# Optimization experiments

Hardware: AMD Instinct MI355X
Metric: run time of the kernel (lower is better)

## Reference

```python
import jax, jax.numpy as jnp
import numpy as np
from jax import lax

KH = KW = 3
STRIDE = 1
PAD = 1
B_COEF = 1.0
IN_CH = 64
OUT_CH = 64
C_LEN = 8
MLP_HIDDEN = 16


def setup_inputs() -> dict:
    key = jax.random.key(0)
    ks = jax.random.split(key, 8)
    IKK = IN_CH * KH * KW
    x = jax.random.normal(ks[0], (2, IN_CH, 32, 32), dtype=jnp.float32)
    c = jax.random.normal(ks[1], (2, C_LEN), dtype=jnp.float32)
    # static kernel [O, I*k*k] (xavier-uniform-ish)
    lim_k = float(np.sqrt(6.0 / (OUT_CH + IKK)))
    kernel = jax.random.uniform(ks[2], (OUT_CH, IKK), minval=-lim_k, maxval=lim_k, dtype=jnp.float32)
    bias = jax.random.normal(ks[3], (OUT_CH,), dtype=jnp.float32)
    # MLP: Linear(2+c_len -> 2*mlp_hidden), SiLU, Linear(2*mlp_hidden -> O*I*k*k)
    d_in = 2 + C_LEN
    d_h = 2 * MLP_HIDDEN
    lim1 = 0.1 * float(np.sqrt(6.0 / (d_in + d_h)))
    lim2 = 0.1 * float(np.sqrt(6.0 / (d_h + OUT_CH * IKK)))
    w1 = jax.random.uniform(ks[4], (d_in, d_h), minval=-lim1, maxval=lim1, dtype=jnp.float32)
    b1 = jnp.zeros((d_h,), dtype=jnp.float32)
    w2 = jax.random.uniform(ks[5], (d_h, OUT_CH * IKK), minval=-lim2, maxval=lim2, dtype=jnp.float32)
    b2 = jnp.zeros((OUT_CH * IKK,), dtype=jnp.float32)
    return {"x": x, "c": c, "kernel": kernel, "bias": bias, "w1": w1, "b1": b1, "w2": w2, "b2": b2}


def reference(x, c, kernel, bias, w1, b1, w2, b2):
    B, C, H, W = x.shape
    Ho = (H + 2 * PAD - KH) // STRIDE + 1
    Wo = (W + 2 * PAD - KW) // STRIDE + 1
    P = Ho * Wo
    O, IKK = kernel.shape
    # unfold: patches feature dim is channel-major (c, kh, kw), matching torch.nn.Unfold
    patches = lax.conv_general_dilated_patches(
        x, (KH, KW), (STRIDE, STRIDE), [(PAD, PAD), (PAD, PAD)])  # [B, IKK, Ho, Wo]
    xu = patches.reshape(B, IKK, P)  # [B, IKK, P]
    # normalized patch locations; ij-meshgrid over (x=W, y=H), flattened x-major (faithful to source)
    gx, gy = jnp.meshgrid(jnp.arange(Wo), jnp.arange(Ho), indexing='ij')
    locs = jnp.stack([gx / Wo, gy / Ho], axis=-1).reshape(-1, 2).astype(x.dtype)  # [P, 2]
    feat = jnp.concatenate(
        [jnp.broadcast_to(locs[None], (B, P, 2)),
         jnp.broadcast_to(c[:, None, :], (B, P, c.shape[1]))], axis=-1
    ).reshape(B * P, -1)  # [B*P, 2+c_len]
    h = jax.nn.silu(feat @ w1 + b1)
    adj = h @ w2 + b2  # [B*P, O*IKK]
    # faithful reshape (same raw-buffer reinterpretation as the torch .view)
    adj = adj.reshape(B, O, P, IKK).transpose(0, 1, 3, 2)  # [B, O, IKK, P]
    ak = kernel[None, :, :, None] + B_COEF * adj  # [B, O, IKK, P]
    out = jnp.einsum('bip,boip->bop', xu, ak)  # [B, O, P]
    out = out + bias[None, :, None]
    return out.reshape(B, O, Ho, Wo)
```

## Files before the change

### kernel.cpp

```cpp
#include <hip/hip_runtime.h>
#include <math.h>

#define CIN   64
#define HH    32
#define WW    32
#define OCH   64
#define IKK   576
#define DH    32
#define OIKK  36864
#define WSTR  296
#define KHALF 288

typedef __attribute__((ext_vector_type(4))) short short4v;
typedef __attribute__((ext_vector_type(8))) short short8v;
typedef __attribute__((ext_vector_type(4))) float f32x4;

__device__ __forceinline__ float silu_f(float v) {
    return v / (1.0f + __expf(-v));
}
__device__ __forceinline__ unsigned short f2bf(float f) {
    unsigned int u = __float_as_uint(f);
    return (unsigned short)((u + 0x7FFFu + ((u >> 16) & 1u)) >> 16);
}
__device__ __forceinline__ float bf2f(unsigned short s) {
    return __uint_as_float(((unsigned int)s) << 16);
}

__global__ __launch_bounds__(512) void k_one(
    const float* __restrict__ x, const float* __restrict__ c,
    const float* __restrict__ kern, const float* __restrict__ bias,
    const float* __restrict__ w1, const float* __restrict__ b1,
    const float* __restrict__ w2, const float* __restrict__ b2,
    float* __restrict__ out)
{
    __shared__ __align__(16) short patch_t[IKK * 16];
    __shared__ __align__(16) short wslab[64 * WSTR];
    __shared__ float t_sm[32][17];
    __shared__ float conv_sm[32][17];
    __shared__ float spart[16][17];
    __shared__ float s_sm[16];

    int tid = threadIdx.x;
    int bid = blockIdx.x;
    int oh  = bid & 1;
    int q   = (bid >> 1) & 63;
    int b   = bid >> 7;
    int par = q >> 5, xq = q & 31;

    for (int idx = tid; idx < 16 * IKK; idx += 512) {
        int pp  = idx / IKK;
        int ikk = idx - pp * IKK;
        int ci  = ikk / 9;
        int r   = ikk - ci * 9;
        int kh  = r / 3;
        int kw  = r - kh * 3;
        int yy  = 2 * pp + par + kh - 1;
        int xx  = xq + kw - 1;
        float v = 0.0f;
        if (yy >= 0 && yy < HH && xx >= 0 && xx < WW)
            v = x[((b * CIN + ci) * HH + yy) * WW + xx];
        patch_t[ikk * 16 + pp] = (short)f2bf(v);
    }

    int srow = tid >> 3;
    int s8   = tid & 7;
    const float* grow = (srow < 32)
        ? (w2   + (size_t)srow * OIKK + q * IKK)
        : (kern + (size_t)((oh << 5) + srow - 32) * IKK);

    {
        const float4* gsrc = (const float4*)(grow) + s8 * 9;
        #pragma unroll
        for (int i = 0; i < 9; ++i) {
            float4 v4 = gsrc[i];
            ushort4 w4 = { f2bf(v4.x), f2bf(v4.y), f2bf(v4.z), f2bf(v4.w) };
            *(ushort4*)&wslab[srow * WSTR + (s8 * 9 + i) * 4] = w4;
        }
    }
    __syncthreads();

    int lane = tid & 63;
    int wid  = tid >> 6;
    int rt   = wid & 3;
    int sub  = wid >> 2;
    int g    = lane >> 4;
    int m    = lane & 15;
    int s_lo = sub ? 5 : 0, s_hi = sub ? 9 : 5;

    f32x4 acc = {0.f, 0.f, 0.f, 0.f};
    unsigned pbase = (unsigned)(size_t)&patch_t[0];

    for (int half = 0; half < 2; ++half) {
        if (half == 1) {
            __syncthreads();
            const float4* gsrc = (const float4*)(grow + KHALF) + s8 * 9;
            #pragma unroll
            for (int i = 0; i < 9; ++i) {
                float4 v4 = gsrc[i];
                ushort4 w4 = { f2bf(v4.x), f2bf(v4.y), f2bf(v4.z), f2bf(v4.w) };
                *(ushort4*)&wslab[srow * WSTR + (s8 * 9 + i) * 4] = w4;
            }
            __syncthreads();
        }
        for (int stp = s_lo; stp < s_hi; ++stp) {
            short8v a = *(const short8v*)&wslab[(rt * 16 + m) * WSTR + stp * 32 + g * 8];
            int krow = half * KHALF + stp * 32 + g * 8 + (m >> 2);
            unsigned baddr = pbase + (unsigned)(krow * 32 + (m & 3) * 8);
            short4v lo, hi;
            asm volatile("ds_read_b64_tr_b16 %0, %1" : "=v"(lo) : "v"(baddr));
            asm volatile("ds_read_b64_tr_b16 %0, %1 offset:128" : "=v"(hi) : "v"(baddr));
            asm volatile("s_waitcnt lgkmcnt(0)" ::: "memory");
            __builtin_amdgcn_sched_barrier(0);
            short8v bfr = { lo[0], lo[1], lo[2], lo[3], hi[0], hi[1], hi[2], hi[3] };
            acc = __builtin_amdgcn_mfma_f32_16x16x32_bf16(a, bfr, acc, 0, 0, 0);
        }
    }
    __syncthreads();

    f32x4* red = (f32x4*)wslab;
    if (sub == 1) {
        red[rt * 64 + lane] = acc;
    } else {
        int px = tid >> 4, kc = tid & 15;
        const float* b2q = b2 + q * IKK + kc * 36;
        float a0 = 0.f;
        #pragma unroll
        for (int i = 0; i < 36; ++i)
            a0 = fmaf(bf2f((unsigned short)patch_t[(kc * 36 + i) * 16 + px]), b2q[i], a0);
        spart[px][kc] = a0;
    }
    __syncthreads();

    if (sub == 0) {
        f32x4 o = red[rt * 64 + lane];
        #pragma unroll
        for (int r = 0; r < 4; ++r) {
            int row = rt * 16 + g * 4 + r;
            float v = acc[r] + o[r];
            if (row < 32) t_sm[row][m] = v;
            else          conv_sm[row - 32][m] = v;
        }
    } else if (rt == 0 && lane < 16) {
        float a0 = 0.f;
        #pragma unroll
        for (int kc = 0; kc < 16; ++kc) a0 += spart[lane][kc];
        s_sm[lane] = a0;
    }
    __syncthreads();

    {
        int o  = tid & 31;
        int p2 = tid >> 5;
        int og = (oh << 5) + o;
        float cb[8];
        #pragma unroll
        for (int i = 0; i < 8; ++i) cb[i] = c[(b << 3) + i];
        int pl = (og << 4) + p2;
        float f0 = (float)(pl >> 5) * (1.0f / 32.0f);
        float f1 = (float)(pl & 31) * (1.0f / 32.0f);
        float dyn = s_sm[p2];
        #pragma unroll 4
        for (int j = 0; j < DH; ++j) {
            float v = b1[j];
            v = fmaf(f0, w1[j], v);
            v = fmaf(f1, w1[DH + j], v);
            #pragma unroll
            for (int i = 0; i < 8; ++i)
                v = fmaf(cb[i], w1[(2 + i) * DH + j], v);
            dyn = fmaf(silu_f(v), t_sm[j][p2], dyn);
        }
        out[((b * OCH + og) << 10) + (p2 << 6) + q] = conv_sm[o][p2] + bias[og] + dyn;
    }
}

extern "C" void kernel_launch(void* const* d_in, const int* in_sizes, int n_in,
                              void* d_out, int out_size, void* d_ws, size_t ws_size,
                              hipStream_t stream) {
    const float* x    = (const float*)d_in[0];
    const float* c    = (const float*)d_in[1];
    const float* kern = (const float*)d_in[2];
    const float* bias = (const float*)d_in[3];
    const float* w1   = (const float*)d_in[4];
    const float* b1   = (const float*)d_in[5];
    const float* w2   = (const float*)d_in[6];
    const float* b2   = (const float*)d_in[7];
    float* out = (float*)d_out;

    k_one<<<256, 512, 0, stream>>>(x, c, kern, bias, w1, b1, w2, b2, out);
}
```

Baseline: 20.68 us.

## Prefetch weight halves into registers to overlap global loads with patch build

Issues the global loads for both halves of the weight slab early, into register arrays. The first half is loaded before the im2col patch construction and the second half after it, so global-memory latency overlaps the patch gather and the first MFMA pass. The patch loop is fully unrolled with incremental index updates instead of per-element division, and the bf16 conversion now uses the HIP intrinsic. This costs more registers (72 extra floats per thread), which with 512-thread blocks may cause spills or lower occupancy.

New measurement: 20.17 us. 1.03x faster.

```diff
diff --git a/kernel.cpp b/kernel.cpp
--- a/kernel.cpp
+++ b/kernel.cpp
@@ -1,4 +1,5 @@
 #include <hip/hip_runtime.h>
+#include <hip/hip_bf16.h>
 #include <math.h>
 
 #define CIN   64
@@ -19,8 +20,8 @@
     return v / (1.0f + __expf(-v));
 }
 __device__ __forceinline__ unsigned short f2bf(float f) {
-    unsigned int u = __float_as_uint(f);
-    return (unsigned short)((u + 0x7FFFu + ((u >> 16) & 1u)) >> 16);
+    __hip_bfloat16 h = __float2bfloat16(f);
+    return *reinterpret_cast<unsigned short*>(&h);
 }
 __device__ __forceinline__ float bf2f(unsigned short s) {
     return __uint_as_float(((unsigned int)s) << 16);
@@ -47,36 +48,45 @@
     int b   = bid >> 7;
     int par = q >> 5, xq = q & 31;
 
-    for (int idx = tid; idx < 16 * IKK; idx += 512) {
-        int pp  = idx / IKK;
-        int ikk = idx - pp * IKK;
-        int ci  = ikk / 9;
-        int r   = ikk - ci * 9;
-        int kh  = r / 3;
-        int kw  = r - kh * 3;
-        int yy  = 2 * pp + par + kh - 1;
-        int xx  = xq + kw - 1;
-        float v = 0.0f;
-        if (yy >= 0 && yy < HH && xx >= 0 && xx < WW)
-            v = x[((b * CIN + ci) * HH + yy) * WW + xx];
-        patch_t[ikk * 16 + pp] = (short)f2bf(v);
-    }
-
     int srow = tid >> 3;
     int s8   = tid & 7;
     const float* grow = (srow < 32)
         ? (w2   + (size_t)srow * OIKK + q * IKK)
         : (kern + (size_t)((oh << 5) + srow - 32) * IKK);
+    const float4* g0 = (const float4*)(grow) + s8 * 9;
+    const float4* g1 = (const float4*)(grow + KHALF) + s8 * 9;
+
+    float4 h0[9];
+    #pragma unroll
+    for (int i = 0; i < 9; ++i) h0[i] = g0[i];
 
     {
-        const float4* gsrc = (const float4*)(grow) + s8 * 9;
-        #pragma unroll
-        for (int i = 0; i < 9; ++i) {
-            float4 v4 = gsrc[i];
-            ushort4 w4 = { f2bf(v4.x), f2bf(v4.y), f2bf(v4.z), f2bf(v4.w) };
-            *(ushort4*)&wslab[srow * WSTR + (s8 * 9 + i) * 4] = w4;
+        int pp = 0, ikk = tid;
+        #pragma unroll
+        for (int it = 0; it < 18; ++it) {
+            int ci = ikk / 9;
+            int r  = ikk - ci * 9;
+            int kh = r / 3;
+            int kw = r - kh * 3;
+            int yy = 2 * pp + par + kh - 1;
+            int xx = xq + kw - 1;
+            float v = 0.0f;
+            if (yy >= 0 && yy < HH && xx >= 0 && xx < WW)
+                v = x[((b * CIN + ci) * HH + yy) * WW + xx];
+            patch_t[ikk * 16 + pp] = (short)f2bf(v);
+            ikk += 512;
+            if (ikk >= IKK) { ikk -= IKK; ++pp; }
         }
     }
+
+    #pragma unroll
+    for (int i = 0; i < 9; ++i) {
+        ushort4 w4 = { f2bf(h0[i].x), f2bf(h0[i].y), f2bf(h0[i].z), f2bf(h0[i].w) };
+        *(ushort4*)&wslab[srow * WSTR + (s8 * 9 + i) * 4] = w4;
+    }
+    float4 h1[9];
+    #pragma unroll
+    for (int i = 0; i < 9; ++i) h1[i] = g1[i];
     __syncthreads();
 
     int lane = tid & 63;
@@ -90,30 +100,38 @@
     f32x4 acc = {0.f, 0.f, 0.f, 0.f};
     unsigned pbase = (unsigned)(size_t)&patch_t[0];
 
-    for (int half = 0; half < 2; ++half) {
-        if (half == 1) {
-            __syncthreads();
-            const float4* gsrc = (const float4*)(grow + KHALF) + s8 * 9;
-            #pragma unroll
-            for (int i = 0; i < 9; ++i) {
-                float4 v4 = gsrc[i];
-                ushort4 w4 = { f2bf(v4.x), f2bf(v4.y), f2bf(v4.z), f2bf(v4.w) };
-                *(ushort4*)&wslab[srow * WSTR + (s8 * 9 + i) * 4] = w4;
-            }
-            __syncthreads();
-        }
-        for (int stp = s_lo; stp < s_hi; ++stp) {
-            short8v a = *(const short8v*)&wslab[(rt * 16 + m) * WSTR + stp * 32 + g * 8];
-            int krow = half * KHALF + stp * 32 + g * 8 + (m >> 2);
-            unsigned baddr = pbase + (unsigned)(krow * 32 + (m & 3) * 8);
-            short4v lo, hi;
-            asm volatile("ds_read_b64_tr_b16 %0, %1" : "=v"(lo) : "v"(baddr));
-            asm volatile("ds_read_b64_tr_b16 %0, %1 offset:128" : "=v"(hi) : "v"(baddr));
-            asm volatile("s_waitcnt lgkmcnt(0)" ::: "memory");
-            __builtin_amdgcn_sched_barrier(0);
-            short8v bfr = { lo[0], lo[1], lo[2], lo[3], hi[0], hi[1], hi[2], hi[3] };
-            acc = __builtin_amdgcn_mfma_f32_16x16x32_bf16(a, bfr, acc, 0, 0, 0);
-        }
+    for (int stp = s_lo; stp < s_hi; ++stp) {
+        short8v a = *(const short8v*)&wslab[(rt * 16 + m) * WSTR + stp * 32 + g * 8];
+        int krow = stp * 32 + g * 8 + (m >> 2);
+        unsigned baddr = pbase + (unsigned)(krow * 32 + (m & 3) * 8);
+        short4v lo, hi;
+        asm volatile("ds_read_b64_tr_b16 %0, %1" : "=v"(lo) : "v"(baddr));
+        asm volatile("ds_read_b64_tr_b16 %0, %1 offset:128" : "=v"(hi) : "v"(baddr));
+        asm volatile("s_waitcnt lgkmcnt(0)" ::: "memory");
+        __builtin_amdgcn_sched_barrier(0);
+        short8v bfr = { lo[0], lo[1], lo[2], lo[3], hi[0], hi[1], hi[2], hi[3] };
+        acc = __builtin_amdgcn_mfma_f32_16x16x32_bf16(a, bfr, acc, 0, 0, 0);
+    }
+    __syncthreads();
+
+    #pragma unroll
+    for (int i = 0; i < 9; ++i) {
+        ushort4 w4 = { f2bf(h1[i].x), f2bf(h1[i].y), f2bf(h1[i].z), f2bf(h1[i].w) };
+        *(ushort4*)&wslab[srow * WSTR + (s8 * 9 + i) * 4] = w4;
+    }
+    __syncthreads();
+
+    for (int stp = s_lo; stp < s_hi; ++stp) {
+        short8v a = *(const short8v*)&wslab[(rt * 16 + m) * WSTR + stp * 32 + g * 8];
+        int krow = KHALF + stp * 32 + g * 8 + (m >> 2);
+        unsigned baddr = pbase + (unsigned)(krow * 32 + (m & 3) * 8);
+        short4v lo, hi;
+        asm volatile("ds_read_b64_tr_b16 %0, %1" : "=v"(lo) : "v"(baddr));
+        asm volatile("ds_read_b64_tr_b16 %0, %1 offset:128" : "=v"(hi) : "v"(baddr));
+        asm volatile("s_waitcnt lgkmcnt(0)" ::: "memory");
+        __builtin_amdgcn_sched_barrier(0);
+        short8v bfr = { lo[0], lo[1], lo[2], lo[3], hi[0], hi[1], hi[2], hi[3] };
+        acc = __builtin_amdgcn_mfma_f32_16x16x32_bf16(a, bfr, acc, 0, 0, 0);
     }
     __syncthreads();
 
```
